# Kernel optimization log

Measured on AMD Instinct MI355X. Metric: run time of the kernel, lower is better.

## Reference

```python
import jax, jax.numpy as jnp
import numpy as np

DIM = 512
NUM_HEADS = 8
HEAD_DIM = DIM // NUM_HEADS
SCALE = HEAD_DIM ** -0.5


def setup_inputs() -> dict:
    key = jax.random.key(0)
    ks = jax.random.split(key, 10)
    B, Sq, Skv = 4, 2048, 2048
    std = DIM ** -0.5
    return {
        "x1": jax.random.normal(ks[0], (B, Sq, DIM), jnp.float32),
        "x2": jax.random.normal(ks[1], (B, Skv, DIM), jnp.float32),
        "Wq": jax.random.normal(ks[2], (DIM, DIM), jnp.float32) * std,
        "bq": jax.random.normal(ks[3], (DIM,), jnp.float32) * 0.02,
        "Wk": jax.random.normal(ks[4], (DIM, DIM), jnp.float32) * std,
        "bk": jax.random.normal(ks[5], (DIM,), jnp.float32) * 0.02,
        "Wv": jax.random.normal(ks[6], (DIM, DIM), jnp.float32) * std,
        "bv": jax.random.normal(ks[7], (DIM,), jnp.float32) * 0.02,
        "Wo": jax.random.normal(ks[8], (DIM, DIM), jnp.float32) * std,
        "bo": jax.random.normal(ks[9], (DIM,), jnp.float32) * 0.02,
    }


def reference(x1, x2, Wq, bq, Wk, bk, Wv, bv, Wo, bo):
    B, Sq, _ = x1.shape
    Skv = x2.shape[1]
    # Linear projections (torch nn.Linear: x @ W.T + b)
    Q = (x1 @ Wq.T + bq).reshape(B, Sq, NUM_HEADS, HEAD_DIM)
    K = (x2 @ Wk.T + bk).reshape(B, Skv, NUM_HEADS, HEAD_DIM)
    V = (x2 @ Wv.T + bv).reshape(B, Skv, NUM_HEADS, HEAD_DIM)
    # [B, H, Sq, Skv]
    attn = jnp.einsum("bqhd,bkhd->bhqk", Q, K) * SCALE
    attn = jax.nn.softmax(attn, axis=-1)  # dropout is identity in eval mode
    out = jnp.einsum("bhqk,bkhd->bqhd", attn, V).reshape(B, Sq, DIM)
    return out @ Wo.T + bo
```

## Files before the change

### kernel.cpp

```cpp
#include <hip/hip_runtime.h>
#include <math.h>

constexpr int kB = 4, kS = 2048, kDim = 512, kNH = 8, kHD = 64;
constexpr float kQScale = 0.18033688011112042f;

using bf16x8 = __attribute__((ext_vector_type(8))) short;
using f32x4  = __attribute__((ext_vector_type(4))) float;
using f32x16 = __attribute__((ext_vector_type(16))) float;

__device__ __forceinline__ unsigned pack_rn(float f0, float f1) {
  unsigned a = __builtin_bit_cast(unsigned, f0) + 0x8000u;
  unsigned b = __builtin_bit_cast(unsigned, f1) + 0x8000u;
  return __builtin_amdgcn_perm(b, a, 0x07060302u);
}
__device__ __forceinline__ unsigned short f2bf_rn(float f) {
  return (unsigned short)((__builtin_bit_cast(unsigned, f) + 0x8000u) >> 16);
}

#define GLDS(gp, lp) __builtin_amdgcn_global_load_lds(                         \
    (const __attribute__((address_space(1))) void*)(gp),                       \
    (__attribute__((address_space(3))) void*)(lp), 16, 0, 0)

__global__ __launch_bounds__(256) void cvt_bf16(
    const float* __restrict__ x1, const float* __restrict__ x2,
    const float* __restrict__ Wq, const float* __restrict__ Wk,
    const float* __restrict__ Wv, const float* __restrict__ Wo,
    unsigned short* __restrict__ x1b, unsigned short* __restrict__ x2b,
    unsigned short* __restrict__ wb) {
  const size_t i = (size_t)blockIdx.x * 256 + threadIdx.x;
  const float* src;
  unsigned short* dst;
  size_t off;
  if (i < 1048576) { src = x1; dst = x1b; off = i; }
  else if (i < 2097152) { src = x2; dst = x2b; off = i - 1048576; }
  else {
    const size_t j = i - 2097152;
    const int seg = (int)(j >> 16);
    src = seg == 0 ? Wq : seg == 1 ? Wk : seg == 2 ? Wv : Wo;
    dst = wb + (size_t)seg * 262144;
    off = j & 65535;
  }
  const float4 v = *(const float4*)(src + off * 4);
  uint2 o;
  o.x = pack_rn(v.x, v.y);
  o.y = pack_rn(v.z, v.w);
  *(uint2*)(dst + off * 4) = o;
}

__global__ __launch_bounds__(256) void qkv_gemm(
    const unsigned short* __restrict__ x1b, const unsigned short* __restrict__ x2b,
    const unsigned short* __restrict__ wb,
    const float* __restrict__ bq, const float* __restrict__ bk,
    const float* __restrict__ bv,
    unsigned short* __restrict__ Qg, unsigned short* __restrict__ Kg,
    unsigned short* __restrict__ Vg) {
  __shared__ __align__(16) short As0[128 * 32], As1[128 * 32];
  __shared__ __align__(16) short Bs0[128 * 32], Bs1[128 * 32];
  const int z = blockIdx.z;
  const unsigned short* X = z ? x2b : x1b;
  const unsigned short* W = wb + (size_t)z * (kDim * kDim);
  const float* bias = (z == 0) ? bq : (z == 1) ? bk : bv;

  const int t = threadIdx.x, lane = t & 63, w = t >> 6;
  const int g = lane >> 4, c = lane & 15;
  const int bm = blockIdx.y * 128, bn = blockIdx.x * 128;
  const int wm = (w >> 1) * 64, wn = (w & 1) * 64;
  const int lr = lane >> 2, lc = (lane & 3) * 8;

  f32x4 acc[4][4] = {};
  for (int k0 = 0; k0 < kDim; k0 += 64) {
    __syncthreads();
#pragma unroll
    for (int i = 0; i < 2; ++i) {
      const int row = i * 64 + w * 16;
      const size_t ga = (size_t)(bm + row + lr) * kDim + k0 + lc;
      const size_t gb = (size_t)(bn + row + lr) * kDim + k0 + lc;
      GLDS(X + ga, As0 + row * 32);
      GLDS(X + ga + 32, As1 + row * 32);
      GLDS(W + gb, Bs0 + row * 32);
      GLDS(W + gb + 32, Bs1 + row * 32);
    }
    __syncthreads();
#pragma unroll
    for (int kk = 0; kk < 2; ++kk) {
      const short* Ap = kk ? As1 : As0;
      const short* Bp = kk ? Bs1 : Bs0;
      bf16x8 af[4], bfr[4];
#pragma unroll
      for (int tm = 0; tm < 4; ++tm) af[tm] = *(const bf16x8*)&Ap[(wm + tm * 16 + c) * 32 + g * 8];
#pragma unroll
      for (int tn = 0; tn < 4; ++tn) bfr[tn] = *(const bf16x8*)&Bp[(wn + tn * 16 + c) * 32 + g * 8];
#pragma unroll
      for (int tm = 0; tm < 4; ++tm)
#pragma unroll
        for (int tn = 0; tn < 4; ++tn)
          acc[tm][tn] = __builtin_amdgcn_mfma_f32_16x16x32_bf16(af[tm], bfr[tn], acc[tm][tn], 0, 0, 0);
    }
  }

#pragma unroll
  for (int tm = 0; tm < 4; ++tm) {
#pragma unroll
    for (int tn = 0; tn < 4; ++tn) {
      const int n = bn + wn + tn * 16 + c;
      const float bb = bias[n];
      const int m0 = bm + wm + tm * 16 + g * 4;
      const float v0 = acc[tm][tn][0] + bb, v1 = acc[tm][tn][1] + bb;
      const float v2 = acc[tm][tn][2] + bb, v3 = acc[tm][tn][3] + bb;
      const int b_ = m0 >> 11, s0 = m0 & 2047;
      const int h_ = n >> 6, d_ = n & 63;
      const int bh = b_ * kNH + h_;
      if (z == 2) {
        uint2 pv;
        pv.x = pack_rn(v0, v1);
        pv.y = pack_rn(v2, v3);
        *(uint2*)(Vg + (((size_t)(bh * kHD + d_)) << 11) + s0) = pv;
      } else {
        const float sc = (z == 0) ? kQScale : 1.0f;
        unsigned short* dst = (z == 0 ? Qg : Kg) + (((size_t)(bh * kS + s0)) << 6) + d_;
        dst[0]   = f2bf_rn(v0 * sc);
        dst[64]  = f2bf_rn(v1 * sc);
        dst[128] = f2bf_rn(v2 * sc);
        dst[192] = f2bf_rn(v3 * sc);
      }
    }
  }
}

__global__ __launch_bounds__(256) void out_gemm(const unsigned short* __restrict__ A,
                                                const unsigned short* __restrict__ Wob,
                                                const float* __restrict__ bias,
                                                float* __restrict__ Y) {
  __shared__ __align__(16) short As0[128 * 32], As1[128 * 32];
  __shared__ __align__(16) short Bs0[64 * 32], Bs1[64 * 32];
  const int t = threadIdx.x, lane = t & 63, w = t >> 6;
  const int g = lane >> 4, c = lane & 15;
  const int bm = blockIdx.y * 128, bn = blockIdx.x * 64;
  const int lr = lane >> 2, lc = (lane & 3) * 8;

  f32x4 acc[2][4] = {};
  for (int k0 = 0; k0 < kDim; k0 += 64) {
    __syncthreads();
#pragma unroll
    for (int i = 0; i < 2; ++i) {
      const int row = i * 64 + w * 16;
      const size_t ga = (size_t)(bm + row + lr) * kDim + k0 + lc;
      GLDS(A + ga, As0 + row * 32);
      GLDS(A + ga + 32, As1 + row * 32);
    }
    {
      const int row = w * 16;
      const size_t gb = (size_t)(bn + row + lr) * kDim + k0 + lc;
      GLDS(Wob + gb, Bs0 + row * 32);
      GLDS(Wob + gb + 32, Bs1 + row * 32);
    }
    __syncthreads();
#pragma unroll
    for (int kk = 0; kk < 2; ++kk) {
      const short* Ap = kk ? As1 : As0;
      const short* Bp = kk ? Bs1 : Bs0;
      bf16x8 af[2], bfr[4];
#pragma unroll
      for (int tm = 0; tm < 2; ++tm) af[tm] = *(const bf16x8*)&Ap[(w * 32 + tm * 16 + c) * 32 + g * 8];
#pragma unroll
      for (int tn = 0; tn < 4; ++tn) bfr[tn] = *(const bf16x8*)&Bp[(tn * 16 + c) * 32 + g * 8];
#pragma unroll
      for (int tm = 0; tm < 2; ++tm)
#pragma unroll
        for (int tn = 0; tn < 4; ++tn)
          acc[tm][tn] = __builtin_amdgcn_mfma_f32_16x16x32_bf16(af[tm], bfr[tn], acc[tm][tn], 0, 0, 0);
    }
  }
#pragma unroll
  for (int tm = 0; tm < 2; ++tm)
#pragma unroll
    for (int tn = 0; tn < 4; ++tn) {
      const int n = bn + tn * 16 + c;
      const float bb = bias[n];
      const int m0 = bm + w * 32 + tm * 16 + g * 4;
#pragma unroll
      for (int r = 0; r < 4; ++r)
        Y[(size_t)(m0 + r) * kDim + n] = acc[tm][tn][r] + bb;
    }
}

__global__ __launch_bounds__(256) void flash_mfma(const unsigned short* __restrict__ Qg,
                                                  const unsigned short* __restrict__ Kg,
                                                  const unsigned short* __restrict__ Vg,
                                                  unsigned short* __restrict__ attn) {
  __shared__ __align__(16) short Ks[64 * 76];
  __shared__ __align__(16) short Vs[64 * 76];
  const int t = threadIdx.x, lane = t & 63, w = t >> 6;
  const int c32 = lane & 31, g2 = lane >> 5;
  const int bh = blockIdx.x, q0 = blockIdx.y * 128, b_ = bh >> 3, h_ = bh & 7;

  const unsigned short* Qp = Qg + ((size_t)bh * kS + q0) * kHD;
  const unsigned short* Kp = Kg + (size_t)bh * kS * kHD;
  const unsigned short* Vp = Vg + (size_t)bh * kHD * kS;

  bf16x8 bq[4];
  {
    const unsigned short* qrow = Qp + (size_t)(w * 32 + c32) * kHD + g2 * 8;
#pragma unroll
    for (int ks = 0; ks < 4; ++ks) bq[ks] = *(const bf16x8*)(qrow + ks * 16);
  }

  const int r0 = t >> 3, cc0 = (t & 7) * 8;
  const int pr = r0 ^ ((((r0 >> 2) ^ (r0 >> 3)) & 1) * 12);
  const unsigned short* kpt = Kp + (size_t)r0 * kHD + cc0;
  const unsigned short* vpt = Vp + (size_t)r0 * kS + cc0;
  uint4 pk0 = *(const uint4*)kpt;
  uint4 pk1 = *(const uint4*)(kpt + 32 * kHD);
  uint4 pv0 = *(const uint4*)vpt;
  uint4 pv1 = *(const uint4*)(vpt + 32 * kS);
  kpt += 64 * kHD;
  vpt += 64;

  float l = 0.f;
  f32x16 o0 = {}, o1 = {};

  for (int kv0 = 0; kv0 < kS; kv0 += 64) {
    __syncthreads();
    *(uint4*)&Ks[pr * 76 + cc0] = pk0;
    *(uint4*)&Ks[(pr + 32) * 76 + cc0] = pk1;
    *(uint4*)&Vs[r0 * 76 + cc0] = pv0;
    *(uint4*)&Vs[(r0 + 32) * 76 + cc0] = pv1;
    if (kv0 + 64 < kS) {
      pk0 = *(const uint4*)kpt;
      pk1 = *(const uint4*)(kpt + 32 * kHD);
      pv0 = *(const uint4*)vpt;
      pv1 = *(const uint4*)(vpt + 32 * kS);
      kpt += 64 * kHD;
      vpt += 64;
    }
    __syncthreads();

    f32x16 sa0 = {}, sa1 = {};
#pragma unroll
    for (int ks = 0; ks < 4; ++ks) {
      const bf16x8 a0 = *(const bf16x8*)&Ks[c32 * 76 + ks * 16 + g2 * 8];
      const bf16x8 a1 = *(const bf16x8*)&Ks[(32 + c32) * 76 + ks * 16 + g2 * 8];
      sa0 = __builtin_amdgcn_mfma_f32_32x32x16_bf16(a0, bq[ks], sa0, 0, 0, 0);
      sa1 = __builtin_amdgcn_mfma_f32_32x32x16_bf16(a1, bq[ks], sa1, 0, 0, 0);
    }

    uint4 bp[4];
#pragma unroll
    for (int kt = 0; kt < 2; ++kt) {
      const f32x16 sv = kt ? sa1 : sa0;
#pragma unroll
      for (int h = 0; h < 2; ++h) {
        float p[8];
#pragma unroll
        for (int j = 0; j < 8; ++j) p[j] = exp2f(sv[h * 8 + j]);
        l += ((p[0] + p[1]) + (p[2] + p[3])) + ((p[4] + p[5]) + (p[6] + p[7]));
        uint4 pk;
        pk.x = pack_rn(p[0], p[1]);
        pk.y = pack_rn(p[2], p[3]);
        pk.z = pack_rn(p[4], p[5]);
        pk.w = pack_rn(p[6], p[7]);
        bp[kt * 2 + h] = pk;
      }
    }

#pragma unroll
    for (int kvs = 0; kvs < 4; ++kvs) {
      const bf16x8 bpf = __builtin_bit_cast(bf16x8, bp[kvs]);
      const bf16x8 v0 = *(const bf16x8*)&Vs[c32 * 76 + kvs * 16 + g2 * 8];
      const bf16x8 v1 = *(const bf16x8*)&Vs[(32 + c32) * 76 + kvs * 16 + g2 * 8];
      o0 = __builtin_amdgcn_mfma_f32_32x32x16_bf16(v0, bpf, o0, 0, 0, 0);
      o1 = __builtin_amdgcn_mfma_f32_32x32x16_bf16(v1, bpf, o1, 0, 0, 0);
    }
  }

  l += __shfl_xor(l, 32, 64);
  const float inv = 1.0f / l;
  unsigned short* orow = attn + ((size_t)b_ * kS + q0 + w * 32 + c32) * kDim + h_ * kHD;
#pragma unroll
  for (int dt = 0; dt < 2; ++dt) {
    const f32x16 oo = dt ? o1 : o0;
#pragma unroll
    for (int rg = 0; rg < 4; ++rg) {
      uint2 st;
      st.x = pack_rn(oo[rg * 4 + 0] * inv, oo[rg * 4 + 1] * inv);
      st.y = pack_rn(oo[rg * 4 + 2] * inv, oo[rg * 4 + 3] * inv);
      *(uint2*)(orow + dt * 32 + 8 * rg + 4 * g2) = st;
    }
  }
}

extern "C" void kernel_launch(void* const* d_in, const int* in_sizes, int n_in,
                              void* d_out, int out_size, void* d_ws, size_t ws_size,
                              hipStream_t stream) {
  const float* x1 = (const float*)d_in[0];
  const float* x2 = (const float*)d_in[1];
  const float* Wq = (const float*)d_in[2];
  const float* bq = (const float*)d_in[3];
  const float* Wk = (const float*)d_in[4];
  const float* bk = (const float*)d_in[5];
  const float* Wv = (const float*)d_in[6];
  const float* bv = (const float*)d_in[7];
  const float* Wo = (const float*)d_in[8];
  const float* bo = (const float*)d_in[9];
  float* out = (float*)d_out;

  constexpr size_t kTok = (size_t)kB * kS * kDim;
  unsigned short* x1b = (unsigned short*)d_ws;
  unsigned short* x2b = x1b + kTok;
  unsigned short* wb  = x2b + kTok;
  unsigned short* Qg  = wb + 4 * (size_t)(kDim * kDim);
  unsigned short* Kg  = Qg + kTok;
  unsigned short* Vg  = Kg + kTok;
  unsigned short* atb = Vg + kTok;

  const dim3 blk(256);
  cvt_bf16<<<dim3(9216), blk, 0, stream>>>(x1, x2, Wq, Wk, Wv, Wo, x1b, x2b, wb);
  qkv_gemm<<<dim3(4, 64, 3), blk, 0, stream>>>(x1b, x2b, wb, bq, bk, bv, Qg, Kg, Vg);
  flash_mfma<<<dim3(32, 16), blk, 0, stream>>>(Qg, Kg, Vg, atb);
  out_gemm<<<dim3(8, 64), blk, 0, stream>>>(atb, wb + 3 * (size_t)(kDim * kDim), bo, out);
}
```

Before: 196.1 us.

## Restructure flash attention to 16x16 MFMA with double-buffered KV and vectorized epilogues

The flash attention kernel now uses 64-query blocks across 1024 workgroups, 16x16x32 MFMA tiles, and double-buffered LDS for K/V, which drops one barrier per iteration and overlaps the next tile's stores with compute. It also uses the hardware exp2 builtin and a launch bound of 4 blocks per CU. The QKV and output GEMMs swap their MFMA operands so each lane holds contiguous output columns, which allows packed 8-byte and float4 stores and vector bias loads. The costs are doubled LDS per block and reloading Q for twice as many blocks.

```diff
diff --git a/kernel.cpp b/kernel.cpp
--- a/kernel.cpp
+++ b/kernel.cpp
@@ -6,7 +6,6 @@
 
 using bf16x8 = __attribute__((ext_vector_type(8))) short;
 using f32x4  = __attribute__((ext_vector_type(4))) float;
-using f32x16 = __attribute__((ext_vector_type(16))) float;
 
 __device__ __forceinline__ unsigned pack_rn(float f0, float f1) {
   unsigned a = __builtin_bit_cast(unsigned, f0) + 0x8000u;
@@ -15,6 +14,13 @@
 }
 __device__ __forceinline__ unsigned short f2bf_rn(float f) {
   return (unsigned short)((__builtin_bit_cast(unsigned, f) + 0x8000u) >> 16);
+}
+__device__ __forceinline__ float fexp2(float x) {
+#if __has_builtin(__builtin_amdgcn_exp2f)
+  return __builtin_amdgcn_exp2f(x);
+#else
+  return exp2f(x);
+#endif
 }
 
 #define GLDS(gp, lp) __builtin_amdgcn_global_load_lds(                         \
@@ -85,43 +91,58 @@
     for (int kk = 0; kk < 2; ++kk) {
       const short* Ap = kk ? As1 : As0;
       const short* Bp = kk ? Bs1 : Bs0;
-      bf16x8 af[4], bfr[4];
-#pragma unroll
-      for (int tm = 0; tm < 4; ++tm) af[tm] = *(const bf16x8*)&Ap[(wm + tm * 16 + c) * 32 + g * 8];
-#pragma unroll
-      for (int tn = 0; tn < 4; ++tn) bfr[tn] = *(const bf16x8*)&Bp[(wn + tn * 16 + c) * 32 + g * 8];
-#pragma unroll
-      for (int tm = 0; tm < 4; ++tm)
-#pragma unroll
-        for (int tn = 0; tn < 4; ++tn)
-          acc[tm][tn] = __builtin_amdgcn_mfma_f32_16x16x32_bf16(af[tm], bfr[tn], acc[tm][tn], 0, 0, 0);
-    }
-  }
-
-#pragma unroll
-  for (int tm = 0; tm < 4; ++tm) {
-#pragma unroll
-    for (int tn = 0; tn < 4; ++tn) {
-      const int n = bn + wn + tn * 16 + c;
-      const float bb = bias[n];
-      const int m0 = bm + wm + tm * 16 + g * 4;
-      const float v0 = acc[tm][tn][0] + bb, v1 = acc[tm][tn][1] + bb;
-      const float v2 = acc[tm][tn][2] + bb, v3 = acc[tm][tn][3] + bb;
-      const int b_ = m0 >> 11, s0 = m0 & 2047;
-      const int h_ = n >> 6, d_ = n & 63;
-      const int bh = b_ * kNH + h_;
+      bf16x8 fa[4], fb[4];
       if (z == 2) {
+#pragma unroll
+        for (int i = 0; i < 4; ++i) fa[i] = *(const bf16x8*)&Ap[(wm + i * 16 + c) * 32 + g * 8];
+#pragma unroll
+        for (int j = 0; j < 4; ++j) fb[j] = *(const bf16x8*)&Bp[(wn + j * 16 + c) * 32 + g * 8];
+      } else {
+#pragma unroll
+        for (int i = 0; i < 4; ++i) fa[i] = *(const bf16x8*)&Bp[(wn + i * 16 + c) * 32 + g * 8];
+#pragma unroll
+        for (int j = 0; j < 4; ++j) fb[j] = *(const bf16x8*)&Ap[(wm + j * 16 + c) * 32 + g * 8];
+      }
+#pragma unroll
+      for (int i = 0; i < 4; ++i)
+#pragma unroll
+        for (int j = 0; j < 4; ++j)
+          acc[i][j] = __builtin_amdgcn_mfma_f32_16x16x32_bf16(fa[i], fb[j], acc[i][j], 0, 0, 0);
+    }
+  }
+
+  if (z == 2) {
+#pragma unroll
+    for (int tm = 0; tm < 4; ++tm)
+#pragma unroll
+      for (int tn = 0; tn < 4; ++tn) {
+        const int n = bn + wn + tn * 16 + c;
+        const float bb = bias[n];
+        const int m0 = bm + wm + tm * 16 + g * 4;
+        const int b_ = m0 >> 11, s0 = m0 & 2047;
+        const int h_ = (n >> 6) & 7, d_ = n & 63;
         uint2 pv;
-        pv.x = pack_rn(v0, v1);
-        pv.y = pack_rn(v2, v3);
-        *(uint2*)(Vg + (((size_t)(bh * kHD + d_)) << 11) + s0) = pv;
-      } else {
-        const float sc = (z == 0) ? kQScale : 1.0f;
-        unsigned short* dst = (z == 0 ? Qg : Kg) + (((size_t)(bh * kS + s0)) << 6) + d_;
-        dst[0]   = f2bf_rn(v0 * sc);
-        dst[64]  = f2bf_rn(v1 * sc);
-        dst[128] = f2bf_rn(v2 * sc);
-        dst[192] = f2bf_rn(v3 * sc);
+        pv.x = pack_rn(acc[tm][tn][0] + bb, acc[tm][tn][1] + bb);
+        pv.y = pack_rn(acc[tm][tn][2] + bb, acc[tm][tn][3] + bb);
+        *(uint2*)(Vg + (((size_t)((b_ * kNH + h_) * kHD + d_)) << 11) + s0) = pv;
+      }
+  } else {
+    const float sc = (z == 0) ? kQScale : 1.0f;
+    unsigned short* Og = z ? Kg : Qg;
+#pragma unroll
+    for (int ti = 0; ti < 4; ++ti) {
+      const int n0 = bn + wn + ti * 16 + g * 4;
+      const float4 bb = *(const float4*)(bias + n0);
+      const int h_ = (n0 >> 6) & 7, d0 = n0 & 63;
+#pragma unroll
+      for (int tj = 0; tj < 4; ++tj) {
+        const int m = bm + wm + tj * 16 + c;
+        const int b_ = m >> 11, s_ = m & 2047;
+        const f32x4 a = acc[ti][tj];
+        uint2 st;
+        st.x = pack_rn((a[0] + bb.x) * sc, (a[1] + bb.y) * sc);
+        st.y = pack_rn((a[2] + bb.z) * sc, (a[3] + bb.w) * sc);
+        *(uint2*)(Og + (((size_t)((b_ * kNH + h_) * kS + s_)) << 6) + d0) = st;
       }
     }
   }
@@ -138,7 +159,7 @@
   const int bm = blockIdx.y * 128, bn = blockIdx.x * 64;
   const int lr = lane >> 2, lc = (lane & 3) * 8;
 
-  f32x4 acc[2][4] = {};
+  f32x4 acc[4][2] = {};
   for (int k0 = 0; k0 < kDim; k0 += 64) {
     __syncthreads();
 #pragma unroll
@@ -159,133 +180,140 @@
     for (int kk = 0; kk < 2; ++kk) {
       const short* Ap = kk ? As1 : As0;
       const short* Bp = kk ? Bs1 : Bs0;
-      bf16x8 af[2], bfr[4];
-#pragma unroll
-      for (int tm = 0; tm < 2; ++tm) af[tm] = *(const bf16x8*)&Ap[(w * 32 + tm * 16 + c) * 32 + g * 8];
-#pragma unroll
-      for (int tn = 0; tn < 4; ++tn) bfr[tn] = *(const bf16x8*)&Bp[(tn * 16 + c) * 32 + g * 8];
-#pragma unroll
-      for (int tm = 0; tm < 2; ++tm)
-#pragma unroll
-        for (int tn = 0; tn < 4; ++tn)
-          acc[tm][tn] = __builtin_amdgcn_mfma_f32_16x16x32_bf16(af[tm], bfr[tn], acc[tm][tn], 0, 0, 0);
-    }
-  }
-#pragma unroll
-  for (int tm = 0; tm < 2; ++tm)
-#pragma unroll
-    for (int tn = 0; tn < 4; ++tn) {
-      const int n = bn + tn * 16 + c;
-      const float bb = bias[n];
-      const int m0 = bm + w * 32 + tm * 16 + g * 4;
-#pragma unroll
-      for (int r = 0; r < 4; ++r)
-        Y[(size_t)(m0 + r) * kDim + n] = acc[tm][tn][r] + bb;
-    }
-}
-
-__global__ __launch_bounds__(256) void flash_mfma(const unsigned short* __restrict__ Qg,
-                                                  const unsigned short* __restrict__ Kg,
-                                                  const unsigned short* __restrict__ Vg,
-                                                  unsigned short* __restrict__ attn) {
-  __shared__ __align__(16) short Ks[64 * 76];
-  __shared__ __align__(16) short Vs[64 * 76];
+      bf16x8 fa[4], fb[2];
+#pragma unroll
+      for (int i = 0; i < 4; ++i) fa[i] = *(const bf16x8*)&Bp[(i * 16 + c) * 32 + g * 8];
+#pragma unroll
+      for (int j = 0; j < 2; ++j) fb[j] = *(const bf16x8*)&Ap[(w * 32 + j * 16 + c) * 32 + g * 8];
+#pragma unroll
+      for (int i = 0; i < 4; ++i)
+#pragma unroll
+        for (int j = 0; j < 2; ++j)
+          acc[i][j] = __builtin_amdgcn_mfma_f32_16x16x32_bf16(fa[i], fb[j], acc[i][j], 0, 0, 0);
+    }
+  }
+#pragma unroll
+  for (int i = 0; i < 4; ++i) {
+    const int n0 = bn + i * 16 + g * 4;
+    const float4 bb = *(const float4*)(bias + n0);
+#pragma unroll
+    for (int j = 0; j < 2; ++j) {
+      const int m = bm + w * 32 + j * 16 + c;
+      float4 st;
+      st.x = acc[i][j][0] + bb.x;
+      st.y = acc[i][j][1] + bb.y;
+      st.z = acc[i][j][2] + bb.z;
+      st.w = acc[i][j][3] + bb.w;
+      *(float4*)(Y + (size_t)m * kDim + n0) = st;
+    }
+  }
+}
+
+__global__ __launch_bounds__(256, 4) void flash_mfma(const unsigned short* __restrict__ Qg,
+                                                     const unsigned short* __restrict__ Kg,
+                                                     const unsigned short* __restrict__ Vg,
+                                                     unsigned short* __restrict__ attn) {
+  __shared__ __align__(16) short Ks[2][64 * 76];
+  __shared__ __align__(16) short Vs[2][64 * 76];
   const int t = threadIdx.x, lane = t & 63, w = t >> 6;
-  const int c32 = lane & 31, g2 = lane >> 5;
-  const int bh = blockIdx.x, q0 = blockIdx.y * 128, b_ = bh >> 3, h_ = bh & 7;
+  const int c = lane & 15, g4 = lane >> 4;
+  const int bh = blockIdx.x, q0 = blockIdx.y * 64;
+  const int b_ = bh >> 3, h_ = bh & 7;
 
   const unsigned short* Qp = Qg + ((size_t)bh * kS + q0) * kHD;
   const unsigned short* Kp = Kg + (size_t)bh * kS * kHD;
   const unsigned short* Vp = Vg + (size_t)bh * kHD * kS;
 
-  bf16x8 bq[4];
+  bf16x8 bq[2];
   {
-    const unsigned short* qrow = Qp + (size_t)(w * 32 + c32) * kHD + g2 * 8;
-#pragma unroll
-    for (int ks = 0; ks < 4; ++ks) bq[ks] = *(const bf16x8*)(qrow + ks * 16);
+    const unsigned short* qr = Qp + (size_t)(w * 16 + c) * kHD + g4 * 8;
+    bq[0] = *(const bf16x8*)qr;
+    bq[1] = *(const bf16x8*)(qr + 32);
   }
 
   const int r0 = t >> 3, cc0 = (t & 7) * 8;
-  const int pr = r0 ^ ((((r0 >> 2) ^ (r0 >> 3)) & 1) * 12);
+  const int ps = (((r0 >> 2) & 1) << 4) | (((r0 >> 3) & 3) << 2) | (r0 & 3);
   const unsigned short* kpt = Kp + (size_t)r0 * kHD + cc0;
   const unsigned short* vpt = Vp + (size_t)r0 * kS + cc0;
-  uint4 pk0 = *(const uint4*)kpt;
-  uint4 pk1 = *(const uint4*)(kpt + 32 * kHD);
-  uint4 pv0 = *(const uint4*)vpt;
-  uint4 pv1 = *(const uint4*)(vpt + 32 * kS);
-  kpt += 64 * kHD;
-  vpt += 64;
+
+  *(uint4*)&Ks[0][ps * 76 + cc0] = *(const uint4*)kpt;
+  *(uint4*)&Ks[0][(ps + 32) * 76 + cc0] = *(const uint4*)(kpt + 32 * kHD);
+  *(uint4*)&Vs[0][r0 * 76 + cc0] = *(const uint4*)vpt;
+  *(uint4*)&Vs[0][(r0 + 32) * 76 + cc0] = *(const uint4*)(vpt + 32 * kS);
+  uint4 pk0 = *(const uint4*)(kpt + 64 * kHD);
+  uint4 pk1 = *(const uint4*)(kpt + 96 * kHD);
+  uint4 pv0 = *(const uint4*)(vpt + 64);
+  uint4 pv1 = *(const uint4*)(vpt + 32 * kS + 64);
+  kpt += 128 * kHD;
+  vpt += 128;
+  __syncthreads();
 
   float l = 0.f;
-  f32x16 o0 = {}, o1 = {};
-
-  for (int kv0 = 0; kv0 < kS; kv0 += 64) {
-    __syncthreads();
-    *(uint4*)&Ks[pr * 76 + cc0] = pk0;
-    *(uint4*)&Ks[(pr + 32) * 76 + cc0] = pk1;
-    *(uint4*)&Vs[r0 * 76 + cc0] = pv0;
-    *(uint4*)&Vs[(r0 + 32) * 76 + cc0] = pv1;
-    if (kv0 + 64 < kS) {
-      pk0 = *(const uint4*)kpt;
-      pk1 = *(const uint4*)(kpt + 32 * kHD);
-      pv0 = *(const uint4*)vpt;
-      pv1 = *(const uint4*)(vpt + 32 * kS);
-      kpt += 64 * kHD;
-      vpt += 64;
-    }
-    __syncthreads();
-
-    f32x16 sa0 = {}, sa1 = {};
-#pragma unroll
-    for (int ks = 0; ks < 4; ++ks) {
-      const bf16x8 a0 = *(const bf16x8*)&Ks[c32 * 76 + ks * 16 + g2 * 8];
-      const bf16x8 a1 = *(const bf16x8*)&Ks[(32 + c32) * 76 + ks * 16 + g2 * 8];
-      sa0 = __builtin_amdgcn_mfma_f32_32x32x16_bf16(a0, bq[ks], sa0, 0, 0, 0);
-      sa1 = __builtin_amdgcn_mfma_f32_32x32x16_bf16(a1, bq[ks], sa1, 0, 0, 0);
-    }
-
-    uint4 bp[4];
-#pragma unroll
-    for (int kt = 0; kt < 2; ++kt) {
-      const f32x16 sv = kt ? sa1 : sa0;
-#pragma unroll
-      for (int h = 0; h < 2; ++h) {
-        float p[8];
-#pragma unroll
-        for (int j = 0; j < 8; ++j) p[j] = exp2f(sv[h * 8 + j]);
-        l += ((p[0] + p[1]) + (p[2] + p[3])) + ((p[4] + p[5]) + (p[6] + p[7]));
-        uint4 pk;
-        pk.x = pack_rn(p[0], p[1]);
-        pk.y = pack_rn(p[2], p[3]);
-        pk.z = pack_rn(p[4], p[5]);
-        pk.w = pack_rn(p[6], p[7]);
-        bp[kt * 2 + h] = pk;
-      }
-    }
-
-#pragma unroll
-    for (int kvs = 0; kvs < 4; ++kvs) {
-      const bf16x8 bpf = __builtin_bit_cast(bf16x8, bp[kvs]);
-      const bf16x8 v0 = *(const bf16x8*)&Vs[c32 * 76 + kvs * 16 + g2 * 8];
-      const bf16x8 v1 = *(const bf16x8*)&Vs[(32 + c32) * 76 + kvs * 16 + g2 * 8];
-      o0 = __builtin_amdgcn_mfma_f32_32x32x16_bf16(v0, bpf, o0, 0, 0, 0);
-      o1 = __builtin_amdgcn_mfma_f32_32x32x16_bf16(v1, bpf, o1, 0, 0, 0);
-    }
-  }
-
+  f32x4 o[4] = {};
+
+#pragma unroll 2
+  for (int it = 0; it < 32; ++it) {
+    const short* Kc = Ks[it & 1];
+    const short* Vc = Vs[it & 1];
+
+    f32x4 sa[4] = {};
+#pragma unroll
+    for (int ks = 0; ks < 2; ++ks)
+#pragma unroll
+      for (int kt = 0; kt < 4; ++kt) {
+        const bf16x8 a = *(const bf16x8*)&Kc[(kt * 16 + c) * 76 + ks * 32 + g4 * 8];
+        sa[kt] = __builtin_amdgcn_mfma_f32_16x16x32_bf16(a, bq[ks], sa[kt], 0, 0, 0);
+      }
+
+    if (it < 31) {
+      short* Kn = Ks[(it + 1) & 1];
+      short* Vn = Vs[(it + 1) & 1];
+      *(uint4*)&Kn[ps * 76 + cc0] = pk0;
+      *(uint4*)&Kn[(ps + 32) * 76 + cc0] = pk1;
+      *(uint4*)&Vn[r0 * 76 + cc0] = pv0;
+      *(uint4*)&Vn[(r0 + 32) * 76 + cc0] = pv1;
+      if (it < 30) {
+        pk0 = *(const uint4*)kpt;
+        pk1 = *(const uint4*)(kpt + 32 * kHD);
+        pv0 = *(const uint4*)vpt;
+        pv1 = *(const uint4*)(vpt + 32 * kS);
+        kpt += 64 * kHD;
+        vpt += 64;
+      }
+    }
+
+#pragma unroll
+    for (int ks = 0; ks < 2; ++ks) {
+      const float p0 = fexp2(sa[2 * ks][0]), p1 = fexp2(sa[2 * ks][1]);
+      const float p2 = fexp2(sa[2 * ks][2]), p3 = fexp2(sa[2 * ks][3]);
+      const float p4 = fexp2(sa[2 * ks + 1][0]), p5 = fexp2(sa[2 * ks + 1][1]);
+      const float p6 = fexp2(sa[2 * ks + 1][2]), p7 = fexp2(sa[2 * ks + 1][3]);
+      l += ((p0 + p1) + (p2 + p3)) + ((p4 + p5) + (p6 + p7));
+      uint4 bp;
+      bp.x = pack_rn(p0, p1);
+      bp.y = pack_rn(p2, p3);
+      bp.z = pack_rn(p4, p5);
+      bp.w = pack_rn(p6, p7);
+      const bf16x8 bpf = __builtin_bit_cast(bf16x8, bp);
+#pragma unroll
+      for (int dt = 0; dt < 4; ++dt) {
+        const bf16x8 va = *(const bf16x8*)&Vc[(dt * 16 + c) * 76 + ks * 32 + g4 * 8];
+        o[dt] = __builtin_amdgcn_mfma_f32_16x16x32_bf16(va, bpf, o[dt], 0, 0, 0);
+      }
+    }
+    __syncthreads();
+  }
+
+  l += __shfl_xor(l, 16, 64);
   l += __shfl_xor(l, 32, 64);
   const float inv = 1.0f / l;
-  unsigned short* orow = attn + ((size_t)b_ * kS + q0 + w * 32 + c32) * kDim + h_ * kHD;
-#pragma unroll
-  for (int dt = 0; dt < 2; ++dt) {
-    const f32x16 oo = dt ? o1 : o0;
-#pragma unroll
-    for (int rg = 0; rg < 4; ++rg) {
-      uint2 st;
-      st.x = pack_rn(oo[rg * 4 + 0] * inv, oo[rg * 4 + 1] * inv);
-      st.y = pack_rn(oo[rg * 4 + 2] * inv, oo[rg * 4 + 3] * inv);
-      *(uint2*)(orow + dt * 32 + 8 * rg + 4 * g2) = st;
-    }
+  unsigned short* orow = attn + ((size_t)(b_ * kS + q0 + w * 16 + c)) * kDim + h_ * kHD;
+#pragma unroll
+  for (int dt = 0; dt < 4; ++dt) {
+    uint2 st;
+    st.x = pack_rn(o[dt][0] * inv, o[dt][1] * inv);
+    st.y = pack_rn(o[dt][2] * inv, o[dt][3] * inv);
+    *(uint2*)(orow + dt * 16 + g4 * 4) = st;
   }
 }
 
@@ -316,6 +344,6 @@
   const dim3 blk(256);
   cvt_bf16<<<dim3(9216), blk, 0, stream>>>(x1, x2, Wq, Wk, Wv, Wo, x1b, x2b, wb);
   qkv_gemm<<<dim3(4, 64, 3), blk, 0, stream>>>(x1b, x2b, wb, bq, bk, bv, Qg, Kg, Vg);
-  flash_mfma<<<dim3(32, 16), blk, 0, stream>>>(Qg, Kg, Vg, atb);
+  flash_mfma<<<dim3(32, 32), blk, 0, stream>>>(Qg, Kg, Vg, atb);
   out_gemm<<<dim3(8, 64), blk, 0, stream>>>(atb, wb + 3 * (size_t)(kDim * kDim), bo, out);
 }
```

New measurement: 394.0 us. 2.01x slower.
